# Kernel optimization log

Measured on AMD Instinct MI355X. Metric: run time of the kernel, lower is better.

## Reference

```python
import jax, jax.numpy as jnp
import numpy as np

B, S, E, H = 2, 2048, 1024, 16
Dh = E // H
LN_EPS = 1e-5


def setup_inputs() -> dict:
    key = jax.random.key(0)
    ks = jax.random.split(key, 12)
    std = 1.0 / np.sqrt(E)
    inp = {
        "query": jax.random.normal(ks[0], (B, S, E), jnp.float32),
        "key":   jax.random.normal(ks[1], (B, S, E), jnp.float32),
        "value": jax.random.normal(ks[2], (B, S, E), jnp.float32),
        # True = masked. Causal mask so every row keeps >=1 valid entry.
        "mask": jnp.broadcast_to(jnp.triu(jnp.ones((S, S), bool), k=1), (B, S, S)),
        # per-head QKV projections, stacked: weight [H, Dh, E] (torch Linear layout), bias [H, Dh]
        "Wq_w": jax.random.uniform(ks[3], (H, Dh, E), jnp.float32, -std, std),
        "Wq_b": jax.random.uniform(ks[4], (H, Dh), jnp.float32, -std, std),
        "Wk_w": jax.random.uniform(ks[5], (H, Dh, E), jnp.float32, -std, std),
        "Wk_b": jax.random.uniform(ks[6], (H, Dh), jnp.float32, -std, std),
        "Wv_w": jax.random.uniform(ks[7], (H, Dh, E), jnp.float32, -std, std),
        "Wv_b": jax.random.uniform(ks[8], (H, Dh), jnp.float32, -std, std),
        # output projection [E, E] (torch layout: out = x @ W.T + b)
        "out_w": jax.random.uniform(ks[9], (E, E), jnp.float32, -std, std),
        "out_b": jax.random.uniform(ks[10], (E,), jnp.float32, -std, std),
        "ln_g": jnp.ones((E,), jnp.float32),
        "ln_b": jnp.zeros((E,), jnp.float32),
    }
    return inp


def reference(query, key, value, mask, Wq_w, Wq_b, Wk_w, Wk_b, Wv_w, Wv_b, out_w, out_b, ln_g, ln_b):
    # per-head projections (batched over heads): [B,S,E] x [H,Dh,E] -> [B,H,S,Dh]
    q = jnp.einsum('bse,hde->bhsd', query, Wq_w) + Wq_b[None, :, None, :]
    k = jnp.einsum('bse,hde->bhsd', key,   Wk_w) + Wk_b[None, :, None, :]
    v = jnp.einsum('bse,hde->bhsd', value, Wv_w) + Wv_b[None, :, None, :]
    scale = 1.0 / np.sqrt(Dh).astype(np.float32)
    scores = jnp.einsum('bhsd,bhtd->bhst', q, k) * scale  # [B,H,S,S]
    scores = jnp.where(mask[:, None, :, :], -jnp.inf, scores)
    probs = jax.nn.softmax(scores, axis=-1)  # dropout p=0 (eval)
    ctx = jnp.einsum('bhst,bhtd->bhsd', probs, v)  # [B,H,S,Dh]
    att = ctx.transpose(0, 2, 1, 3).reshape(query.shape[0], query.shape[1], -1)  # concat heads [B,S,E]
    proj = att @ out_w.T + out_b  # dropout p=0
    x = query + proj  # residual
    mu = jnp.mean(x, axis=-1, keepdims=True)
    var = jnp.mean(jnp.square(x - mu), axis=-1, keepdims=True)
    return (x - mu) * jax.lax.rsqrt(var + LN_EPS) * ln_g + ln_b
```

## Files before the change

kernel.cpp:

```cpp
#include <hip/hip_runtime.h>
#include <stdint.h>

#define B_ 2
#define S_ 2048
#define E_ 1024
#define H_ 16
#define DH 64
#define M_TOT (B_*S_)

typedef short s16x8 __attribute__((ext_vector_type(8)));
typedef float f32x4 __attribute__((ext_vector_type(4)));
typedef unsigned int u32;
typedef unsigned short u16;

union V8 { uint4 u; s16x8 v; };

__device__ __forceinline__ u32 fbits(float f){ union{float f;u32 i;}x; x.f=f; return x.i; }
__device__ __forceinline__ u32 prround(float f){ return fbits(f)+0x8000u; }
__device__ __forceinline__ u16 f2bf(float f){ return (u16)(prround(f)>>16); }
__device__ __forceinline__ u32 permpack(u32 hi,u32 lo){ return __builtin_amdgcn_perm(hi,lo,0x07060302u); }
__device__ __forceinline__ uint4 pack8r(const float4 a, const float4 b){
    uint4 p;
    p.x = permpack(prround(a.y),prround(a.x));
    p.y = permpack(prround(a.w),prround(a.z));
    p.z = permpack(prround(b.y),prround(b.x));
    p.w = permpack(prround(b.w),prround(b.z));
    return p;
}
__device__ __forceinline__ float exp2_fast(float x){ float r; asm("v_exp_f32 %0, %1":"=v"(r):"v"(x)); return r; }

typedef const __attribute__((address_space(1))) u32* gas_t;
typedef __attribute__((address_space(3))) u32* las_t;
#define GLDS16(gp, lp) __builtin_amdgcn_global_load_lds((gas_t)(gp), (las_t)(lp), 16, 0, 0)

__global__ __launch_bounds__(256) void cvtw(
    const float* __restrict__ w0, const float* __restrict__ w1, const float* __restrict__ w2,
    u16* __restrict__ dst, int n4)
{
    const int z = blockIdx.y;
    const float* s = (z==0)?w0:(z==1)?w1:w2;
    u16* d = dst + (size_t)z*E_*E_;
    int i = blockIdx.x*256 + threadIdx.x;
    const int stride = gridDim.x*256;
    for (; i<n4; i+=stride){
        float4 v = ((const float4*)s)[i];
        uint2 p;
        p.x = permpack(prround(v.y),prround(v.x));
        p.y = permpack(prround(v.w),prround(v.z));
        ((uint2*)d)[i] = p;
    }
}
__global__ __launch_bounds__(256) void cvt1(
    const float* __restrict__ s, u16* __restrict__ d, int n4)
{
    int i = blockIdx.x*256 + threadIdx.x;
    const int stride = gridDim.x*256;
    for (; i<n4; i+=stride){
        float4 v = ((const float4*)s)[i];
        uint2 p;
        p.x = permpack(prround(v.y),prround(v.x));
        p.y = permpack(prround(v.w),prround(v.z));
        ((uint2*)d)[i] = p;
    }
}

__global__ __launch_bounds__(256) void qkv128(
    const float* __restrict__ xq, const float* __restrict__ xk, const float* __restrict__ xv,
    const u16* __restrict__ Wb,
    const float* __restrict__ bq, const float* __restrict__ bk, const float* __restrict__ bv,
    u16* __restrict__ oq, u16* __restrict__ ok_, u16* __restrict__ ovt)
{
    const int bid = blockIdx.x;
    const int c = bid & 7;
    const int t = bid >> 3;
    const int n = t & 7;
    const int g = ((t >> 3) << 3) + c;
    const int m = g & 31, z = g >> 5;

    const float* X = (z==0)?xq:(z==1)?xk:xv;
    const u16* W = Wb + (size_t)z*E_*E_;
    const float* bia = (z==0)?bq:(z==1)?bk:bv;
    const float scale = (z==0)? 0.125f*1.44269504f : 1.0f;

    __shared__ __align__(16) u16 As[128*40];
    __shared__ __align__(16) u16 Bs[128*32];

    const int tid = threadIdx.x;
    const int wid = tid>>6, lane = tid&63;
    const int lrow = lane&15, quad = lane>>4;
    const int ldr = tid>>2, ldc = (tid&3)*8;
    const int mb = m*128, nb = n*128;
    const int wm = (wid>>1)*64, wn = (wid&1)*64;
    const int brow = lane>>2, bkq = lane&3;

    f32x4 acc[4][4] = {};
    const float* Xrow = X + (size_t)(mb+ldr)*E_ + ldc;
    const u16*  Wn = W + (size_t)nb*E_;

    for (int k0=0;k0<E_;k0+=32){
        const float4 fa0 = *(const float4*)(Xrow + k0);
        const float4 fa1 = *(const float4*)(Xrow + k0 + 4);
        const float4 fb0 = *(const float4*)(Xrow + (size_t)64*E_ + k0);
        const float4 fb1 = *(const float4*)(Xrow + (size_t)64*E_ + k0 + 4);
        __syncthreads();
        *(uint4*)&As[ldr*40 + ldc] = pack8r(fa0, fa1);
        *(uint4*)&As[(ldr+64)*40 + ldc] = pack8r(fb0, fb1);
#pragma unroll
        for (int i=0;i<2;i++){
            const int rb = wid*32 + i*16;
            GLDS16(Wn + (size_t)(rb+brow)*E_ + k0 + (bkq<<3), &Bs[rb*32]);
        }
        __syncthreads();

        s16x8 af[4], bfr[4];
#pragma unroll
        for (int mi=0;mi<4;mi++) af[mi] = *(const s16x8*)&As[(wm+mi*16+lrow)*40 + quad*8];
#pragma unroll
        for (int ci=0;ci<4;ci++) bfr[ci] = *(const s16x8*)&Bs[(wn+ci*16+lrow)*32 + quad*8];
#pragma unroll
        for (int mi=0;mi<4;mi++)
#pragma unroll
            for (int ci=0;ci<4;ci++)
                acc[mi][ci] = __builtin_amdgcn_mfma_f32_16x16x32_bf16(af[mi], bfr[ci], acc[mi][ci],0,0,0);
    }

    if (z < 2){
        u16* O = (z==0)?oq:ok_;
#pragma unroll
        for (int ci=0;ci<4;ci++){
            const int nn = nb+wn+ci*16+lrow;
            const float bval = bia[nn];
            const int h = nn>>6, d = nn&63;
#pragma unroll
            for (int mi=0;mi<4;mi++){
#pragma unroll
                for (int r=0;r<4;r++){
                    const int mm = mb+wm+mi*16+quad*4+r;
                    const int bb = mm>>11, s = mm&(S_-1);
                    O[(((size_t)(bb*H_+h))*S_+s)*DH + d] = f2bf((acc[mi][ci][r]+bval)*scale);
                }
            }
        }
    } else {
#pragma unroll
        for (int ci=0;ci<4;ci++){
            const int nn = nb+wn+ci*16+lrow;
            const float bval = bia[nn];
            const int h = nn>>6, d = nn&63;
#pragma unroll
            for (int mi=0;mi<4;mi++){
                const int m0 = mb+wm+mi*16+quad*4;
                const int bb = m0>>11, s0 = m0&(S_-1);
                uint2 pk;
                pk.x = permpack(prround(acc[mi][ci][1]+bval), prround(acc[mi][ci][0]+bval));
                pk.y = permpack(prround(acc[mi][ci][3]+bval), prround(acc[mi][ci][2]+bval));
                *(uint2*)&ovt[(((size_t)(bb*H_+h))*DH + d)*S_ + s0] = pk;
            }
        }
    }
}

__global__ __launch_bounds__(256) void attn(
    const u16* __restrict__ q_ws, const u16* __restrict__ k_ws,
    const u16* __restrict__ vt_ws, u16* __restrict__ att)
{
    const int bid = blockIdx.x;
    const int c8 = bid & 7;
    const int t = bid >> 3;
    const int p = t & 15;
    const int bh = ((t >> 4) << 3) + c8;
    const int b = bh>>4, h = bh&15;

    const u16* Qb = q_ws + (size_t)bh*S_*DH;
    const u16* Kb = k_ws + (size_t)bh*S_*DH;
    const u16* VT = vt_ws + (size_t)bh*DH*S_;

    __shared__ __align__(16) u16 Ks[64*64];
    __shared__ __align__(16) u16 Vt[64*64];
    __shared__ __align__(16) u16 Ps[4][16*64];

    const int tid = threadIdx.x;
    const int wid = tid>>6, lane = tid&63;
    const int lrow = lane&15, quad = lane>>4;
    u16* Pw = Ps[wid];

    const int srw = lane>>3;
    const int scs = lane&7;
    const int sgc = scs ^ srw;

    for (int ph=0; ph<2; ph++){
        const int qi = ph ? (31-p) : p;
        const int qb = qi<<6;

        s16x8 qf[2];
#pragma unroll
        for (int ch=0;ch<2;ch++)
            qf[ch] = *(const s16x8*)&Qb[(size_t)(qb+wid*16+lrow)*DH + ch*32 + quad*8];

        f32x4 o[4] = {};
        float l_lane = 0.f;
        const int qglob = qb + wid*16 + lrow;
        const int ntile = qi + 1;

        for (int ti=0; ti<ntile; ti++){
            const int t0 = ti<<6;
            __syncthreads();
#pragma unroll
            for (int g=0; g<2; g++){
                const int rg = wid*16 + g*8 + srw;
                GLDS16(Kb + (size_t)(t0+rg)*DH + (sgc<<3), &Ks[(wid*16+g*8)*64]);
                GLDS16(VT + (size_t)rg*S_ + t0 + (sgc<<3), &Vt[(wid*16+g*8)*64]);
            }
            __syncthreads();

            f32x4 st[4] = {};
#pragma unroll
            for (int tt=0;tt<4;tt++){
                const int tr = tt*16+lrow;
#pragma unroll
                for (int ch=0;ch<2;ch++){
                    const int slot = (ch*4+quad) ^ (lrow&7);
                    const s16x8 kf = *(const s16x8*)&Ks[tr*64 + slot*8];
                    st[tt] = __builtin_amdgcn_mfma_f32_16x16x32_bf16(kf, qf[ch], st[tt],0,0,0);
                }
            }

            if (ti == ntile-1){
#pragma unroll
                for (int tt=0;tt<4;tt++){
                    const int tg = t0 + tt*16 + quad*4;
#pragma unroll
                    for (int r=0;r<4;r++)
                        if (tg + r > qglob) st[tt][r] = -1e30f;
                }
            }

#pragma unroll
            for (int tt=0;tt<4;tt++){
                const float p0 = exp2_fast(st[tt][0]);
                const float p1 = exp2_fast(st[tt][1]);
                const float p2 = exp2_fast(st[tt][2]);
                const float p3 = exp2_fast(st[tt][3]);
                l_lane += (p0+p1)+(p2+p3);
                const int tc = tt*2 + (quad>>1);
                const int ts = tc ^ (lrow&7);
                const int a0 = lrow*64 + ts*8 + (quad&1)*4;
                *(u32*)&Pw[a0]   = permpack(prround(p1),prround(p0));
                *(u32*)&Pw[a0+2] = permpack(prround(p3),prround(p2));
            }

            s16x8 pb[2];
#pragma unroll
            for (int ch=0;ch<2;ch++){
                const int slot = (ch*4+quad) ^ (lrow&7);
                pb[ch] = *(const s16x8*)&Pw[lrow*64 + slot*8];
            }

#pragma unroll
            for (int cc=0;cc<4;cc++){
                const int vr = cc*16+lrow;
#pragma unroll
                for (int ch=0;ch<2;ch++){
                    const int slot = (ch*4+quad) ^ (lrow&7);
                    const s16x8 vf = *(const s16x8*)&Vt[vr*64 + slot*8];
                    o[cc] = __builtin_amdgcn_mfma_f32_16x16x32_bf16(vf, pb[ch], o[cc],0,0,0);
                }
            }
        }

        float s = l_lane;
        s += __shfl_xor(s, 16, 64);
        s += __shfl_xor(s, 32, 64);
        const float rl = 1.0f/s;

#pragma unroll
        for (int cc=0;cc<4;cc++){
            uint2 pk;
            pk.x = permpack(prround(o[cc][1]*rl), prround(o[cc][0]*rl));
            pk.y = permpack(prround(o[cc][3]*rl), prround(o[cc][2]*rl));
            *(uint2*)&att[(size_t)(b*S_ + qglob)*E_ + h*DH + cc*16 + quad*4] = pk;
        }
    }
}

__global__ __launch_bounds__(256) void oproj128(
    const u16* __restrict__ A, const u16* __restrict__ W, const float* __restrict__ bias,
    const float* __restrict__ resid, float* __restrict__ out)
{
    const int bid = blockIdx.x;
    const int c = bid & 7;
    const int t = bid >> 3;
    const int n = t & 7;
    const int m = ((t >> 3) << 3) + c;

    __shared__ __align__(16) u16 As[128*32];
    __shared__ __align__(16) u16 Bs[128*32];

    const int tid = threadIdx.x;
    const int wid = tid>>6, lane = tid&63;
    const int lrow = lane&15, quad = lane>>4;
    const int mb = m*128, nb = n*128;
    const int wm = (wid>>1)*64, wn = (wid&1)*64;
    const int brow = lane>>2, bkq = lane&3;

    f32x4 acc[4][4] = {};
    const u16* Ab = A + (size_t)mb*E_;
    const u16* Wn = W + (size_t)nb*E_;

    for (int k0=0;k0<E_;k0+=32){
        __syncthreads();
#pragma unroll
        for (int i=0;i<2;i++){
            const int rb = wid*32 + i*16;
            GLDS16(Ab + (size_t)(rb+brow)*E_ + k0 + (bkq<<3), &As[rb*32]);
            GLDS16(Wn + (size_t)(rb+brow)*E_ + k0 + (bkq<<3), &Bs[rb*32]);
        }
        __syncthreads();

        s16x8 af[4], bfr[4];
#pragma unroll
        for (int mi=0;mi<4;mi++) af[mi] = *(const s16x8*)&As[(wm+mi*16+lrow)*32 + quad*8];
#pragma unroll
        for (int ci=0;ci<4;ci++) bfr[ci] = *(const s16x8*)&Bs[(wn+ci*16+lrow)*32 + quad*8];
#pragma unroll
        for (int mi=0;mi<4;mi++)
#pragma unroll
            for (int ci=0;ci<4;ci++)
                acc[mi][ci] = __builtin_amdgcn_mfma_f32_16x16x32_bf16(af[mi], bfr[ci], acc[mi][ci],0,0,0);
    }

#pragma unroll
    for (int ci=0;ci<4;ci++){
        const int nn = nb+wn+ci*16+lrow;
        const float bval = bias[nn];
#pragma unroll
        for (int mi=0;mi<4;mi++){
#pragma unroll
            for (int r=0;r<4;r++){
                const int mm = mb+wm+mi*16+quad*4+r;
                out[(size_t)mm*E_+nn] = acc[mi][ci][r] + bval + resid[(size_t)mm*E_+nn];
            }
        }
    }
}

__global__ __launch_bounds__(256) void ln_k(
    const float* __restrict__ xin, const float* __restrict__ lg,
    const float* __restrict__ lb, float* __restrict__ out)
{
    const int row = blockIdx.x;
    const int tid = threadIdx.x;
    const int wid = tid>>6, lane = tid&63;
    const float* xr = xin + (size_t)row*E_;

    float x[4];
    float s = 0.f;
#pragma unroll
    for (int i=0;i<4;i++){ const int e = i*256+tid; x[i] = xr[e]; s += x[i]; }
    __shared__ float red[8];
#pragma unroll
    for (int off=32; off>0; off>>=1) s += __shfl_xor(s, off, 64);
    if (lane==0) red[wid] = s;
    __syncthreads();
    const float mu = (red[0]+red[1]+red[2]+red[3]) * (1.f/E_);

    float v = 0.f;
#pragma unroll
    for (int i=0;i<4;i++){ const float d = x[i]-mu; v += d*d; }
#pragma unroll
    for (int off=32; off>0; off>>=1) v += __shfl_xor(v, off, 64);
    if (lane==0) red[wid+4] = v;
    __syncthreads();
    const float var = (red[4]+red[5]+red[6]+red[7]) * (1.f/E_);
    const float rs = rsqrtf(var + 1e-5f);

#pragma unroll
    for (int i=0;i<4;i++){
        const int e = i*256+tid;
        out[(size_t)row*E_+e] = (x[i]-mu)*rs*lg[e] + lb[e];
    }
}

extern "C" void kernel_launch(void* const* d_in, const int* in_sizes, int n_in,
                              void* d_out, int out_size, void* d_ws, size_t ws_size,
                              hipStream_t stream) {
    const float* q_in = (const float*)d_in[0];
    const float* k_in = (const float*)d_in[1];
    const float* v_in = (const float*)d_in[2];
    const float* wq = (const float*)d_in[4];
    const float* bq = (const float*)d_in[5];
    const float* wk = (const float*)d_in[6];
    const float* bk = (const float*)d_in[7];
    const float* wv = (const float*)d_in[8];
    const float* bv = (const float*)d_in[9];
    const float* ow = (const float*)d_in[10];
    const float* ob = (const float*)d_in[11];
    const float* lg = (const float*)d_in[12];
    const float* lb = (const float*)d_in[13];
    float* out = (float*)d_out;

    char* ws = (char*)d_ws;
    const size_t MB = (size_t)1<<20;
    u16* q_ws  = (u16*)(ws);
    u16* k_ws  = (u16*)(ws +  8*MB);
    u16* vt_ws = (u16*)(ws + 16*MB);
    u16* att   = (u16*)(ws + 24*MB);
    u16* Wbf   = (u16*)(ws + 24*MB);
    u16* owbf  = (u16*)(ws + 16*MB);
    float* proj = (float*)ws;

    cvtw<<<dim3(512,3), 256, 0, stream>>>(wq, wk, wv, Wbf, (E_*E_)/4);
    qkv128<<<dim3(768), 256, 0, stream>>>(
        q_in, k_in, v_in, Wbf, bq, bk, bv, q_ws, k_ws, vt_ws);
    attn<<<dim3(512), 256, 0, stream>>>(q_ws, k_ws, vt_ws, att);
    cvt1<<<dim3(1024), 256, 0, stream>>>(ow, owbf, (E_*E_)/4);
    oproj128<<<dim3(256), 256, 0, stream>>>(att, owbf, ob, q_in, proj);
    ln_k<<<dim3(M_TOT), 256, 0, stream>>>(proj, lg, lb, out);
}
```

Baseline: 290.7 us.

## Double-buffer LDS staging in QKV, attention and output projection kernels

Adds ping-pong shared-memory buffers to the QKV GEMM, the attention KV loop and the output projection, so the async global-to-LDS load of the next tile overlaps MFMA work on the current one. The QKV kernel now stages raw fp32 activations into LDS with an XOR swizzle and converts them to bf16 when building fragments, instead of converting in registers before the store. The output projection switches to 128x64 tiles with a 512-block grid to raise occupancy and parallelism. In exchange it uses more LDS per block, which may lower occupancy, and it repeats the bf16 conversion for every fragment read.

```diff
diff --git a/kernel.cpp b/kernel.cpp
--- a/kernel.cpp
+++ b/kernel.cpp
@@ -82,46 +82,64 @@
     const float* bia = (z==0)?bq:(z==1)?bk:bv;
     const float scale = (z==0)? 0.125f*1.44269504f : 1.0f;
 
-    __shared__ __align__(16) u16 As[128*40];
-    __shared__ __align__(16) u16 Bs[128*32];
+    __shared__ __align__(16) float As0[128*32];
+    __shared__ __align__(16) float As1[128*32];
+    __shared__ __align__(16) u16  Bs0[128*32];
+    __shared__ __align__(16) u16  Bs1[128*32];
 
     const int tid = threadIdx.x;
     const int wid = tid>>6, lane = tid&63;
     const int lrow = lane&15, quad = lane>>4;
-    const int ldr = tid>>2, ldc = (tid&3)*8;
     const int mb = m*128, nb = n*128;
     const int wm = (wid>>1)*64, wn = (wid&1)*64;
+    const int arow = lane>>3, akq = lane&7;
     const int brow = lane>>2, bkq = lane&3;
 
     f32x4 acc[4][4] = {};
-    const float* Xrow = X + (size_t)(mb+ldr)*E_ + ldc;
+    const float* Xb = X + (size_t)mb*E_;
     const u16*  Wn = W + (size_t)nb*E_;
 
-    for (int k0=0;k0<E_;k0+=32){
-        const float4 fa0 = *(const float4*)(Xrow + k0);
-        const float4 fa1 = *(const float4*)(Xrow + k0 + 4);
-        const float4 fb0 = *(const float4*)(Xrow + (size_t)64*E_ + k0);
-        const float4 fb1 = *(const float4*)(Xrow + (size_t)64*E_ + k0 + 4);
-        __syncthreads();
-        *(uint4*)&As[ldr*40 + ldc] = pack8r(fa0, fa1);
-        *(uint4*)&As[(ldr+64)*40 + ldc] = pack8r(fb0, fb1);
+    auto stage = [&](float* Ad, u16* Bd, int k0){
+#pragma unroll
+        for (int i=0;i<4;i++){
+            const int rb = wid*32 + i*8;
+            GLDS16(Xb + (size_t)(rb+arow)*E_ + k0 + ((akq^arow)<<2), Ad + rb*32);
+        }
 #pragma unroll
         for (int i=0;i<2;i++){
             const int rb = wid*32 + i*16;
-            GLDS16(Wn + (size_t)(rb+brow)*E_ + k0 + (bkq<<3), &Bs[rb*32]);
-        }
-        __syncthreads();
-
+            GLDS16(Wn + (size_t)(rb+brow)*E_ + k0 + (bkq<<3), Bd + rb*32);
+        }
+    };
+    auto compute = [&](const float* Ad, const u16* Bd){
         s16x8 af[4], bfr[4];
 #pragma unroll
-        for (int mi=0;mi<4;mi++) af[mi] = *(const s16x8*)&As[(wm+mi*16+lrow)*40 + quad*8];
-#pragma unroll
-        for (int ci=0;ci<4;ci++) bfr[ci] = *(const s16x8*)&Bs[(wn+ci*16+lrow)*32 + quad*8];
+        for (int mi=0;mi<4;mi++){
+            const int row = wm+mi*16+lrow;
+            const int sw = lrow&7;
+            const float4 fa = *(const float4*)&Ad[row*32 + (((quad<<1)   )^sw)*4];
+            const float4 fb = *(const float4*)&Ad[row*32 + (((quad<<1)|1 )^sw)*4];
+            V8 tt; tt.u = pack8r(fa, fb);
+            af[mi] = tt.v;
+        }
+#pragma unroll
+        for (int ci=0;ci<4;ci++)
+            bfr[ci] = *(const s16x8*)&Bd[(wn+ci*16+lrow)*32 + quad*8];
 #pragma unroll
         for (int mi=0;mi<4;mi++)
 #pragma unroll
             for (int ci=0;ci<4;ci++)
                 acc[mi][ci] = __builtin_amdgcn_mfma_f32_16x16x32_bf16(af[mi], bfr[ci], acc[mi][ci],0,0,0);
+    };
+
+    stage(As0, Bs0, 0);
+    for (int k0=0; k0<E_; k0+=64){
+        __syncthreads();
+        if (k0+32 < E_) stage(As1, Bs1, k0+32);
+        compute(As0, Bs0);
+        __syncthreads();
+        if (k0+64 < E_) stage(As0, Bs0, k0+64);
+        compute(As1, Bs1);
     }
 
     if (z < 2){
@@ -175,8 +193,10 @@
     const u16* Kb = k_ws + (size_t)bh*S_*DH;
     const u16* VT = vt_ws + (size_t)bh*DH*S_;
 
-    __shared__ __align__(16) u16 Ks[64*64];
-    __shared__ __align__(16) u16 Vt[64*64];
+    __shared__ __align__(16) u16 Ks0[64*64];
+    __shared__ __align__(16) u16 Ks1[64*64];
+    __shared__ __align__(16) u16 Vt0[64*64];
+    __shared__ __align__(16) u16 Vt1[64*64];
     __shared__ __align__(16) u16 Ps[4][16*64];
 
     const int tid = threadIdx.x;
@@ -188,6 +208,15 @@
     const int scs = lane&7;
     const int sgc = scs ^ srw;
 
+    auto stageKV = [&](u16* Kd, u16* Vd, int t0){
+#pragma unroll
+        for (int g2=0; g2<2; g2++){
+            const int rg = wid*16 + g2*8 + srw;
+            GLDS16(Kb + (size_t)(t0+rg)*DH + (sgc<<3), Kd + (wid*16+g2*8)*64);
+            GLDS16(VT + (size_t)rg*S_ + t0 + (sgc<<3), Vd + (wid*16+g2*8)*64);
+        }
+    };
+
     for (int ph=0; ph<2; ph++){
         const int qi = ph ? (31-p) : p;
         const int qb = qi<<6;
@@ -202,17 +231,7 @@
         const int qglob = qb + wid*16 + lrow;
         const int ntile = qi + 1;
 
-        for (int ti=0; ti<ntile; ti++){
-            const int t0 = ti<<6;
-            __syncthreads();
-#pragma unroll
-            for (int g=0; g<2; g++){
-                const int rg = wid*16 + g*8 + srw;
-                GLDS16(Kb + (size_t)(t0+rg)*DH + (sgc<<3), &Ks[(wid*16+g*8)*64]);
-                GLDS16(VT + (size_t)rg*S_ + t0 + (sgc<<3), &Vt[(wid*16+g*8)*64]);
-            }
-            __syncthreads();
-
+        auto computeTile = [&](const u16* Kd, const u16* Vd, int t0, bool diag){
             f32x4 st[4] = {};
 #pragma unroll
             for (int tt=0;tt<4;tt++){
@@ -220,12 +239,11 @@
 #pragma unroll
                 for (int ch=0;ch<2;ch++){
                     const int slot = (ch*4+quad) ^ (lrow&7);
-                    const s16x8 kf = *(const s16x8*)&Ks[tr*64 + slot*8];
+                    const s16x8 kf = *(const s16x8*)&Kd[tr*64 + slot*8];
                     st[tt] = __builtin_amdgcn_mfma_f32_16x16x32_bf16(kf, qf[ch], st[tt],0,0,0);
                 }
             }
-
-            if (ti == ntile-1){
+            if (diag){
 #pragma unroll
                 for (int tt=0;tt<4;tt++){
                     const int tg = t0 + tt*16 + quad*4;
@@ -234,7 +252,6 @@
                         if (tg + r > qglob) st[tt][r] = -1e30f;
                 }
             }
-
 #pragma unroll
             for (int tt=0;tt<4;tt++){
                 const float p0 = exp2_fast(st[tt][0]);
@@ -248,24 +265,35 @@
                 *(u32*)&Pw[a0]   = permpack(prround(p1),prround(p0));
                 *(u32*)&Pw[a0+2] = permpack(prround(p3),prround(p2));
             }
-
             s16x8 pb[2];
 #pragma unroll
             for (int ch=0;ch<2;ch++){
                 const int slot = (ch*4+quad) ^ (lrow&7);
                 pb[ch] = *(const s16x8*)&Pw[lrow*64 + slot*8];
             }
-
 #pragma unroll
             for (int cc=0;cc<4;cc++){
                 const int vr = cc*16+lrow;
 #pragma unroll
                 for (int ch=0;ch<2;ch++){
                     const int slot = (ch*4+quad) ^ (lrow&7);
-                    const s16x8 vf = *(const s16x8*)&Vt[vr*64 + slot*8];
+                    const s16x8 vf = *(const s16x8*)&Vd[vr*64 + slot*8];
                     o[cc] = __builtin_amdgcn_mfma_f32_16x16x32_bf16(vf, pb[ch], o[cc],0,0,0);
                 }
             }
+        };
+
+        __syncthreads();
+        stageKV(Ks0, Vt0, 0);
+        for (int ti=0; ; ti+=2){
+            __syncthreads();
+            if (ti+1 < ntile) stageKV(Ks1, Vt1, (ti+1)<<6);
+            computeTile(Ks0, Vt0, ti<<6, ti==ntile-1);
+            if (ti+1 >= ntile) break;
+            __syncthreads();
+            if (ti+2 < ntile) stageKV(Ks0, Vt0, (ti+2)<<6);
+            computeTile(Ks1, Vt1, (ti+1)<<6, ti+1==ntile-1);
+            if (ti+2 >= ntile) break;
         }
 
         float s = l_lane;
@@ -290,54 +318,66 @@
     const int bid = blockIdx.x;
     const int c = bid & 7;
     const int t = bid >> 3;
-    const int n = t & 7;
-    const int m = ((t >> 3) << 3) + c;
-
-    __shared__ __align__(16) u16 As[128*32];
-    __shared__ __align__(16) u16 Bs[128*32];
+    const int n = t & 15;
+    const int m = ((t >> 4) << 3) + c;
+
+    __shared__ __align__(16) u16 As0[128*32];
+    __shared__ __align__(16) u16 As1[128*32];
+    __shared__ __align__(16) u16 Bs0[64*32];
+    __shared__ __align__(16) u16 Bs1[64*32];
 
     const int tid = threadIdx.x;
     const int wid = tid>>6, lane = tid&63;
     const int lrow = lane&15, quad = lane>>4;
-    const int mb = m*128, nb = n*128;
-    const int wm = (wid>>1)*64, wn = (wid&1)*64;
-    const int brow = lane>>2, bkq = lane&3;
-
-    f32x4 acc[4][4] = {};
+    const int mb = m*128, nb = n*64;
+    const int srow = lane>>2, skq = lane&3;
+
+    f32x4 acc[2][4] = {};
     const u16* Ab = A + (size_t)mb*E_;
     const u16* Wn = W + (size_t)nb*E_;
 
-    for (int k0=0;k0<E_;k0+=32){
-        __syncthreads();
+    auto stage = [&](u16* Ad, u16* Bd, int k0){
 #pragma unroll
         for (int i=0;i<2;i++){
             const int rb = wid*32 + i*16;
-            GLDS16(Ab + (size_t)(rb+brow)*E_ + k0 + (bkq<<3), &As[rb*32]);
-            GLDS16(Wn + (size_t)(rb+brow)*E_ + k0 + (bkq<<3), &Bs[rb*32]);
-        }
-        __syncthreads();
-
-        s16x8 af[4], bfr[4];
-#pragma unroll
-        for (int mi=0;mi<4;mi++) af[mi] = *(const s16x8*)&As[(wm+mi*16+lrow)*32 + quad*8];
-#pragma unroll
-        for (int ci=0;ci<4;ci++) bfr[ci] = *(const s16x8*)&Bs[(wn+ci*16+lrow)*32 + quad*8];
-#pragma unroll
-        for (int mi=0;mi<4;mi++)
+            GLDS16(Ab + (size_t)(rb+srow)*E_ + k0 + (skq<<3), Ad + rb*32);
+        }
+        GLDS16(Wn + (size_t)(wid*16+srow)*E_ + k0 + (skq<<3), Bd + (wid*16)*32);
+    };
+    auto compute = [&](const u16* Ad, const u16* Bd){
+        s16x8 af[2], bfr[4];
+#pragma unroll
+        for (int mi=0;mi<2;mi++)
+            af[mi] = *(const s16x8*)&Ad[(wid*32+mi*16+lrow)*32 + quad*8];
+#pragma unroll
+        for (int ci=0;ci<4;ci++)
+            bfr[ci] = *(const s16x8*)&Bd[(ci*16+lrow)*32 + quad*8];
+#pragma unroll
+        for (int mi=0;mi<2;mi++)
 #pragma unroll
             for (int ci=0;ci<4;ci++)
                 acc[mi][ci] = __builtin_amdgcn_mfma_f32_16x16x32_bf16(af[mi], bfr[ci], acc[mi][ci],0,0,0);
+    };
+
+    stage(As0, Bs0, 0);
+    for (int k0=0; k0<E_; k0+=64){
+        __syncthreads();
+        if (k0+32 < E_) stage(As1, Bs1, k0+32);
+        compute(As0, Bs0);
+        __syncthreads();
+        if (k0+64 < E_) stage(As0, Bs0, k0+64);
+        compute(As1, Bs1);
     }
 
 #pragma unroll
     for (int ci=0;ci<4;ci++){
-        const int nn = nb+wn+ci*16+lrow;
+        const int nn = nb+ci*16+lrow;
         const float bval = bias[nn];
 #pragma unroll
-        for (int mi=0;mi<4;mi++){
+        for (int mi=0;mi<2;mi++){
 #pragma unroll
             for (int r=0;r<4;r++){
-                const int mm = mb+wm+mi*16+quad*4+r;
+                const int mm = mb+wid*32+mi*16+quad*4+r;
                 out[(size_t)mm*E_+nn] = acc[mi][ci][r] + bval + resid[(size_t)mm*E_+nn];
             }
         }
@@ -414,6 +454,6 @@
         q_in, k_in, v_in, Wbf, bq, bk, bv, q_ws, k_ws, vt_ws);
     attn<<<dim3(512), 256, 0, stream>>>(q_ws, k_ws, vt_ws, att);
     cvt1<<<dim3(1024), 256, 0, stream>>>(ow, owbf, (E_*E_)/4);
-    oproj128<<<dim3(256), 256, 0, stream>>>(att, owbf, ob, q_in, proj);
+    oproj128<<<dim3(512), 256, 0, stream>>>(att, owbf, ob, q_in, proj);
     ln_k<<<dim3(M_TOT), 256, 0, stream>>>(proj, lg, lb, out);
 }
```

After: 270.9 us. -6.8%, faster.
